# Optimization experiments

Hardware: AMD Instinct MI355X
Metric: run time of the kernel (lower is better)

Reference implementation:

```python
import math
import jax, jax.numpy as jnp
import numpy as np

B_SZ, N_TOK, D_INNER, S_STATE = 4, 1024, 384, 16
DT_MAX = 0.15


def setup_inputs() -> dict:
    key = jax.random.key(0)
    ks = jax.random.split(key, 10)
    dt_init = math.log(math.exp(0.1) - 1.0)  # softplus^-1(0.1)
    x = jax.random.normal(ks[0], (B_SZ, N_TOK, D_INNER), dtype=jnp.float32)
    dt_self_W = jax.random.uniform(ks[1], (D_INNER, D_INNER), minval=-1e-4, maxval=1e-4)
    dt_self_b = jnp.full((D_INNER,), dt_init, dtype=jnp.float32)
    dt_diff_W = jax.random.uniform(ks[2], (D_INNER, D_INNER), minval=-1e-4, maxval=1e-4)
    dt_diff_b = jnp.full((D_INNER,), dt_init, dtype=jnp.float32)
    B_W = jax.random.normal(ks[3], (D_INNER, S_STATE)) / math.sqrt(D_INNER)
    C_real_W = jax.random.normal(ks[4], (D_INNER, S_STATE)) / math.sqrt(D_INNER)
    C_imag_W = jax.random.normal(ks[5], (D_INNER, S_STATE)) / math.sqrt(D_INNER)
    D_param = jnp.ones((D_INNER,), dtype=jnp.float32)
    A_log = jnp.broadcast_to(jnp.log(jnp.arange(1, S_STATE + 1, dtype=jnp.float32))[None, :], (D_INNER, S_STATE))
    lap = jnp.array([[0.0, 1.0, 0.0], [1.0, -4.0, 1.0], [0.0, 1.0, 0.0]], dtype=jnp.float32) * 0.1
    conv_w = jnp.broadcast_to(lap[None, None], (D_INNER, 1, 3, 3)) + 0.01 * jax.random.normal(ks[6], (D_INNER, 1, 3, 3))
    reaction_alpha = 0.01 * jax.random.normal(ks[7], (1, 1, D_INNER, 1))
    reaction_beta = 0.01 * jax.random.normal(ks[8], (1, 1, D_INNER, 1))
    return {
        'x': x, 'dt_self_W': dt_self_W, 'dt_self_b': dt_self_b,
        'dt_diff_W': dt_diff_W, 'dt_diff_b': dt_diff_b,
        'B_W': B_W, 'C_real_W': C_real_W, 'C_imag_W': C_imag_W,
        'D_param': D_param, 'A_log': A_log, 'conv_w': conv_w,
        'reaction_alpha': reaction_alpha, 'reaction_beta': reaction_beta,
        'K_steps': 2,
    }


def _laplacian(h, conv_w, H, W):
    # h: (B, N, D, S) -> depthwise 3x3 conv with replicate pad over the HxW grid
    B, N, D, S = h.shape
    hs = h.transpose(0, 3, 2, 1).reshape(B * S, D, H, W)
    hp = jnp.pad(hs, ((0, 0), (0, 0), (1, 1), (1, 1)), mode='edge')
    lap = jax.lax.conv_general_dilated(
        hp, conv_w, window_strides=(1, 1), padding='VALID',
        feature_group_count=D, dimension_numbers=('NCHW', 'OIHW', 'NCHW'))
    return lap.reshape(B, S, D, N).transpose(0, 3, 2, 1)


def reference(x, dt_self_W, dt_self_b, dt_diff_W, dt_diff_b, B_W, C_real_W,
              C_imag_W, D_param, A_log, conv_w, reaction_alpha, reaction_beta,
              K_steps):
    B, N, D = x.shape
    H = Wg = int(math.sqrt(N))
    A = -jax.nn.softplus(A_log)  # (D, S)
    delta_s = jnp.minimum(jax.nn.softplus(x @ dt_self_W.T + dt_self_b), DT_MAX)[..., None]
    delta_d = jnp.minimum(jax.nn.softplus(x @ dt_diff_W.T + dt_diff_b), DT_MAX)[..., None]
    B_mat = x @ B_W          # (B, N, S)
    C_real = x @ C_real_W    # (B, N, S)
    C_imag = x @ C_imag_W    # (B, N, S)
    mamba_input = jnp.einsum('bnd,bns->bnds', x, B_mat)
    h_real = mamba_input
    h_imag = jnp.zeros_like(h_real)
    dt = 1.0 / K_steps
    A_exp = A[None, None]  # (1,1,D,S)
    for _ in range(K_steps):
        f1_real = delta_s * (A_exp * h_real + mamba_input)
        f1_imag = delta_s * (A_exp * h_imag)
        lap_real = _laplacian(h_real, conv_w, H, Wg)
        lap_imag = _laplacian(h_imag, conv_w, H, Wg)
        f2_real = delta_d * -lap_imag
        f2_imag = delta_d * lap_real
        reaction_scale = reaction_alpha - reaction_beta * (h_real ** 2 + h_imag ** 2)
        h_real = h_real + dt * (f1_real + f2_real + h_real * reaction_scale)
        h_imag = h_imag + dt * (f1_imag + f2_imag + h_imag * reaction_scale)
    y = (jnp.einsum('bnds,bns->bnd', h_real, C_real)
         + jnp.einsum('bnds,bns->bnd', h_imag, C_imag)
         + x * D_param)
    return y
```

## Files before the change

kernel.cpp:

```cpp
#include <hip/hip_runtime.h>
#include <hip/hip_fp16.h>
#include <math.h>

#define B_SZ    4
#define N_TOKC  1024
#define D_INNER 384
#define S_STATE 16
#define DT_MAX_V 0.15f
#define PLANE   (B_SZ * N_TOKC)
#define DN      ((size_t)B_SZ * D_INNER * N_TOKC)

typedef __attribute__((ext_vector_type(8))) short bf16x8;
typedef __attribute__((ext_vector_type(4))) float f32x4;

__device__ __forceinline__ float softplusf(float z) {
    return fmaxf(z, 0.f) + log1pf(expf(-fabsf(z)));
}

__device__ __forceinline__ unsigned short f2bf(float f) {
    unsigned u = __float_as_uint(f);
    unsigned r = (u + 0x7FFFu + ((u >> 16) & 1u)) >> 16;
    return (unsigned short)r;
}

__device__ __forceinline__ unsigned packh2(float a, float b) {
    __half2 h = __floats2half2_rn(a, b);
    union { __half2 h; unsigned u; } c; c.h = h; return c.u;
}
__device__ __forceinline__ __half2 uph2(unsigned u) {
    union { unsigned u; __half2 h; } c; c.u = u; return c.h;
}

__device__ __forceinline__ size_t frag_off(int T, int kb, int q, int l16) {
    return ((size_t)((T * 12 + kb) * 4 + q)) * 128 + l16 * 8;
}

__device__ __forceinline__ bf16x8 pack8(const float* v) {
    bf16x8 o;
#pragma unroll
    for (int e = 0; e < 8; e++) o[e] = (short)f2bf(v[e]);
    return o;
}

__global__ __launch_bounds__(256) void k_prep(
    const float* __restrict__ x, const float* __restrict__ Ws, const float* __restrict__ Wd,
    const float* __restrict__ BW, const float* __restrict__ CrW, const float* __restrict__ CiW,
    const float* __restrict__ A_log,
    float* __restrict__ x_t, unsigned short* __restrict__ xp,
    unsigned short* __restrict__ Wdtp, unsigned short* __restrict__ Wbcp,
    float* __restrict__ A_tab)
{
    const int t = threadIdx.x;
    const int bx = blockIdx.x;
    if (bx < 1536) {
        __shared__ __align__(16) float tile[32][36];
        const int tok0 = (bx & 127) * 32;
        const int d0   = (bx >> 7) * 32;
        const int b = tok0 >> 10, n0 = tok0 & 1023;
        {
            const int r = t >> 3, c4 = (t & 7) * 4;
            const float4 v = *(const float4*)(x + (size_t)(tok0 + r) * D_INNER + d0 + c4);
            tile[r][c4 + 0] = v.x; tile[r][c4 + 1] = v.y;
            tile[r][c4 + 2] = v.z; tile[r][c4 + 3] = v.w;
        }
        __syncthreads();
        {
            const int dr = t >> 3, n4 = (t & 7) * 4;
            float4 o;
            o.x = tile[n4 + 0][dr]; o.y = tile[n4 + 1][dr];
            o.z = tile[n4 + 2][dr]; o.w = tile[n4 + 3][dr];
            *(float4*)(x_t + ((size_t)(b * D_INNER + d0 + dr)) * N_TOKC + n0 + n4) = o;
        }
        if (t < 128) {
            const int tt = t >> 6, q = (t >> 4) & 3, l16 = t & 15;
            const int row = tt * 16 + l16;
            float v[8];
#pragma unroll
            for (int e = 0; e < 8; e++) v[e] = tile[row][q * 8 + e];
            *(bf16x8*)(xp + frag_off((tok0 >> 4) + tt, d0 >> 5, q, l16)) = pack8(v);
        }
    } else if (bx < 1584) {
        const int vv = bx - 1536;
        const int mat = vv >= 24;
        const int dt16 = mat ? vv - 24 : vv;
        const float* W = mat ? Wd : Ws;
        unsigned short* dst = Wdtp + (size_t)mat * 147456;
#pragma unroll
        for (int it = 0; it < 3; it++) {
            const int item = t + it * 256;
            const int l16 = item & 15, q = (item >> 4) & 3, kb = item >> 6;
            const float* src = W + (size_t)(dt16 * 16 + l16) * D_INNER + kb * 32 + q * 8;
            float v[8];
            const float4 v0 = *(const float4*)(src);
            const float4 v1 = *(const float4*)(src + 4);
            v[0] = v0.x; v[1] = v0.y; v[2] = v0.z; v[3] = v0.w;
            v[4] = v1.x; v[5] = v1.y; v[6] = v1.z; v[7] = v1.w;
            *(bf16x8*)(dst + frag_off(dt16, kb, q, l16)) = pack8(v);
        }
    } else if (bx < 1587) {
        const int m = bx - 1584;
        const float* W2 = (m == 0) ? BW : ((m == 1) ? CrW : CiW);
#pragma unroll
        for (int it = 0; it < 3; it++) {
            const int item = t + it * 256;
            const int l16 = item & 15, q = (item >> 4) & 3, kb = item >> 6;
            float v[8];
#pragma unroll
            for (int e = 0; e < 8; e++)
                v[e] = W2[(size_t)(kb * 32 + q * 8 + e) * S_STATE + l16];
            *(bf16x8*)(Wbcp + (size_t)m * 6144 + frag_off(0, kb, q, l16)) = pack8(v);
        }
    } else {
        for (int i = t; i < D_INNER * S_STATE; i += 256)
            A_tab[i] = -softplusf(A_log[i]);
    }
}

__global__ __launch_bounds__(256) void k_gemm(
    const unsigned short* __restrict__ xp, const unsigned short* __restrict__ Wdtp,
    const unsigned short* __restrict__ Wbcp,
    const float* __restrict__ bs, const float* __restrict__ bd,
    float* __restrict__ ds_t, float* __restrict__ dd_t,
    float* __restrict__ Bm_t, float* __restrict__ Cr_t, float* __restrict__ Ci_t)
{
    const int wave = threadIdx.x >> 6;
    const int lane = threadIdx.x & 63;
    const int quad = lane >> 4, l16 = lane & 15;

    if (blockIdx.x < 384) {
        const int dbase = (blockIdx.x >> 6) * 64;
        const int tbase = (blockIdx.x & 63) * 64;
        const int wd = (wave & 1) * 32;
        const int wt = (wave >> 1) * 32;
        const int dT0 = (dbase + wd) >> 4;
        const int tT0 = (tbase + wt) >> 4;

        f32x4 acc[2][2][2];
#pragma unroll
        for (int m = 0; m < 2; m++)
#pragma unroll
            for (int i = 0; i < 2; i++)
#pragma unroll
                for (int j = 0; j < 2; j++) acc[m][i][j] = (f32x4)0.f;

        bf16x8 a0[2][2], b0[2];
#pragma unroll
        for (int m = 0; m < 2; m++)
#pragma unroll
            for (int i = 0; i < 2; i++)
                a0[m][i] = *(const bf16x8*)(Wdtp + (size_t)m * 147456
                                            + frag_off(dT0 + i, 0, quad, l16));
#pragma unroll
        for (int j = 0; j < 2; j++)
            b0[j] = *(const bf16x8*)(xp + frag_off(tT0 + j, 0, quad, l16));

#pragma unroll 2
        for (int kb = 0; kb < 12; kb++) {
            bf16x8 a1[2][2], b1[2];
            const int kn = (kb < 11) ? kb + 1 : 11;
#pragma unroll
            for (int m = 0; m < 2; m++)
#pragma unroll
                for (int i = 0; i < 2; i++)
                    a1[m][i] = *(const bf16x8*)(Wdtp + (size_t)m * 147456
                                                + frag_off(dT0 + i, kn, quad, l16));
#pragma unroll
            for (int j = 0; j < 2; j++)
                b1[j] = *(const bf16x8*)(xp + frag_off(tT0 + j, kn, quad, l16));

#pragma unroll
            for (int m = 0; m < 2; m++)
#pragma unroll
                for (int i = 0; i < 2; i++)
#pragma unroll
                    for (int j = 0; j < 2; j++)
                        acc[m][i][j] = __builtin_amdgcn_mfma_f32_16x16x32_bf16(
                            a0[m][i], b0[j], acc[m][i][j], 0, 0, 0);

#pragma unroll
            for (int m = 0; m < 2; m++)
#pragma unroll
                for (int i = 0; i < 2; i++) a0[m][i] = a1[m][i];
#pragma unroll
            for (int j = 0; j < 2; j++) b0[j] = b1[j];
        }

#pragma unroll
        for (int m = 0; m < 2; m++) {
            const float* bias = (m == 0) ? bs : bd;
            float* out = (m == 0) ? ds_t : dd_t;
#pragma unroll
            for (int i = 0; i < 2; i++)
#pragma unroll
                for (int j = 0; j < 2; j++) {
                    const int tok = tbase + wt + j * 16 + l16;
                    const int bb = tok >> 10, n = tok & 1023;
#pragma unroll
                    for (int reg = 0; reg < 4; reg++) {
                        const int d = dbase + wd + i * 16 + quad * 4 + reg;
                        const float v = fminf(softplusf(acc[m][i][j][reg] + bias[d]), DT_MAX_V);
                        out[((size_t)(bb * D_INNER + d)) * N_TOKC + n] = v;
                    }
                }
        }
    } else {
        const int tT = (blockIdx.x - 384) * 4 + wave;
        f32x4 acc[3];
#pragma unroll
        for (int m = 0; m < 3; m++) acc[m] = (f32x4)0.f;

#pragma unroll 1
        for (int kb = 0; kb < 12; kb++) {
            const bf16x8 b = *(const bf16x8*)(xp + frag_off(tT, kb, quad, l16));
#pragma unroll
            for (int m = 0; m < 3; m++) {
                const bf16x8 a = *(const bf16x8*)(Wbcp + (size_t)m * 6144
                                                  + frag_off(0, kb, quad, l16));
                acc[m] = __builtin_amdgcn_mfma_f32_16x16x32_bf16(a, b, acc[m], 0, 0, 0);
            }
        }

        const int tok = tT * 16 + l16;
#pragma unroll
        for (int m = 0; m < 3; m++) {
            float* plane = (m == 0) ? Bm_t : ((m == 1) ? Cr_t : Ci_t);
#pragma unroll
            for (int reg = 0; reg < 4; reg++) {
                const int s = quad * 4 + reg;
                plane[(size_t)s * PLANE + tok] = acc[m][reg];
            }
        }
    }
}

#define PSTRIDE 33
#define PSIZE   (PSTRIDE * 32)

__global__ __launch_bounds__(256) void k_ssm(
    const float* __restrict__ x_t, const float* __restrict__ conv_w, const float* __restrict__ A_tab,
    const float* __restrict__ ralpha, const float* __restrict__ rbeta, const float* __restrict__ Dp,
    const float* __restrict__ ds_t, const float* __restrict__ dd_t,
    const float* __restrict__ Bm_t, const float* __restrict__ Cr_t, const float* __restrict__ Ci_t,
    float* __restrict__ y_part)
{
    const int sg = blockIdx.x;
    const int d  = blockIdx.y;
    const int b  = blockIdx.z;
    const int t  = threadIdx.x;
    const int c  = t & 31;
    const int g  = t >> 5;
    const int r0 = g * 4;

    __shared__ unsigned pl[4 * PSIZE];

    __half2 wh[9];
#pragma unroll
    for (int i = 0; i < 9; i++) wh[i] = __float2half2_rn(conv_w[d * 9 + i]);
    const float alpha = ralpha[d];
    const float beta  = rbeta[d];
    const float Dv    = Dp[d];
    float A[4];
#pragma unroll
    for (int s = 0; s < 4; s++) A[s] = A_tab[d * S_STATE + sg * 4 + s];

    const size_t base_dn = ((size_t)(b * D_INNER + d)) * N_TOKC;
    const size_t base_sn = (size_t)b * N_TOKC;

    float xv[4], dsv[4], ddv[4], u[4][4];
    float hr[4][4], hi[4][4];
#pragma unroll
    for (int k = 0; k < 4; k++) {
        const int n = (r0 + k) * 32 + c;
        xv[k]  = x_t [base_dn + n];
        dsv[k] = ds_t[base_dn + n];
        ddv[k] = dd_t[base_dn + n];
#pragma unroll
        for (int s = 0; s < 4; s++) {
            u[k][s]  = xv[k] * Bm_t[(size_t)(sg * 4 + s) * PLANE + base_sn + n];
            hr[k][s] = u[k][s];
        }
    }

    int tapw[6][3];
    {
        const int cm = (c > 0)  ? c - 1 : 0;
        const int cp = (c < 31) ? c + 1 : 31;
        const int rtop = (r0 > 0)  ? r0 - 1 : 0;
        const int rbot = (r0 < 28) ? r0 + 4 : 31;
        int rowb[6];
        rowb[0] = rtop * PSTRIDE;
#pragma unroll
        for (int k = 0; k < 4; k++) rowb[k + 1] = (r0 + k) * PSTRIDE;
        rowb[5] = rbot * PSTRIDE;
#pragma unroll
        for (int rr = 0; rr < 6; rr++) {
            tapw[rr][0] = rowb[rr] + cm;
            tapw[rr][1] = rowb[rr] + c;
            tapw[rr][2] = rowb[rr] + cp;
        }
    }
    const int ws0 = r0 * PSTRIDE + c;

#pragma unroll
    for (int p = 0; p < 2; p++)
#pragma unroll
        for (int k = 0; k < 4; k++)
            pl[p * PSIZE + ws0 + k * PSTRIDE] = packh2(hr[k][2 * p], hr[k][2 * p + 1]);
    __syncthreads();

#pragma unroll
    for (int p = 0; p < 2; p++) {
        __half2 tp[6][3];
#pragma unroll
        for (int rr = 0; rr < 6; rr++)
#pragma unroll
            for (int j = 0; j < 3; j++)
                tp[rr][j] = uph2(pl[p * PSIZE + tapw[rr][j]]);
#pragma unroll
        for (int k = 0; k < 4; k++) {
            __half2 ac = __float2half2_rn(0.f);
#pragma unroll
            for (int a = 0; a < 3; a++)
#pragma unroll
                for (int j = 0; j < 3; j++)
                    ac = __hfma2(wh[a * 3 + j], tp[k + a][j], ac);
            const float lap[2] = { __low2float(ac), __high2float(ac) };
#pragma unroll
            for (int e = 0; e < 2; e++) {
                const int s = 2 * p + e;
                const float hrv = hr[k][s];
                const float f1r = dsv[k] * fmaf(A[s], hrv, u[k][s]);
                const float rs  = fmaf(-beta, hrv * hrv, alpha);
                hr[k][s] = hrv + 0.5f * (f1r + hrv * rs);
                hi[k][s] = 0.5f * ddv[k] * lap[e];
            }
        }
    }
    __syncthreads();

#pragma unroll
    for (int s = 0; s < 4; s++)
#pragma unroll
        for (int k = 0; k < 4; k++)
            pl[s * PSIZE + ws0 + k * PSTRIDE] = packh2(hr[k][s], hi[k][s]);
    __syncthreads();

    float yp[4] = { 0.f, 0.f, 0.f, 0.f };
#pragma unroll
    for (int s = 0; s < 4; s++) {
        float crv[4], civ[4];
#pragma unroll
        for (int k = 0; k < 4; k++) {
            const size_t po = (size_t)(sg * 4 + s) * PLANE + base_sn + (r0 + k) * 32 + c;
            crv[k] = Cr_t[po];
            civ[k] = Ci_t[po];
        }
        __half2 tp[6][3];
#pragma unroll
        for (int rr = 0; rr < 6; rr++)
#pragma unroll
            for (int j = 0; j < 3; j++)
                tp[rr][j] = uph2(pl[s * PSIZE + tapw[rr][j]]);
#pragma unroll
        for (int k = 0; k < 4; k++) {
            __half2 ac = __float2half2_rn(0.f);
#pragma unroll
            for (int a = 0; a < 3; a++)
#pragma unroll
                for (int j = 0; j < 3; j++)
                    ac = __hfma2(wh[a * 3 + j], tp[k + a][j], ac);
            const float lapr = __low2float(ac);
            const float lapi = __high2float(ac);
            const float hrv = hr[k][s], hiv = hi[k][s];
            const float f1r = dsv[k] * fmaf(A[s], hrv, u[k][s]);
            const float f1i = dsv[k] * (A[s] * hiv);
            const float f2r = -ddv[k] * lapi;
            const float f2i =  ddv[k] * lapr;
            const float q   = fmaf(hrv, hrv, hiv * hiv);
            const float rs  = fmaf(-beta, q, alpha);
            const float nhr = hrv + 0.5f * (f1r + f2r + hrv * rs);
            const float nhi = hiv + 0.5f * (f1i + f2i + hiv * rs);
            yp[k] = fmaf(nhr, crv[k], yp[k]);
            yp[k] = fmaf(nhi, civ[k], yp[k]);
        }
    }

#pragma unroll
    for (int k = 0; k < 4; k++) {
        float v = yp[k];
        if (sg == 0) v = fmaf(xv[k], Dv, v);
        y_part[((size_t)((sg * B_SZ + b) * D_INNER + d)) * N_TOKC + (r0 + k) * 32 + c] = v;
    }
}

__global__ __launch_bounds__(256) void k_reduce(
    const float* __restrict__ y_part, float* __restrict__ y)
{
    const int d0 = blockIdx.x * 32;
    const int n0 = blockIdx.y * 32;
    const int b  = blockIdx.z;
    const int t  = threadIdx.x;
    __shared__ __align__(16) float tile[32][36];

    const int dr = t >> 3, nc4 = (t & 7) * 4;
    float4 acc = make_float4(0.f, 0.f, 0.f, 0.f);
#pragma unroll
    for (int sg = 0; sg < 4; sg++) {
        const float4 v = *(const float4*)(y_part
            + ((size_t)((sg * B_SZ + b) * D_INNER + d0 + dr)) * N_TOKC + n0 + nc4);
        acc.x += v.x; acc.y += v.y; acc.z += v.z; acc.w += v.w;
    }
    *(float4*)&tile[dr][nc4] = acc;
    __syncthreads();

    const int nr = t >> 3, dc4 = (t & 7) * 4;
    float4 o;
    o.x = tile[dc4 + 0][nr];
    o.y = tile[dc4 + 1][nr];
    o.z = tile[dc4 + 2][nr];
    o.w = tile[dc4 + 3][nr];
    *(float4*)(y + ((size_t)(b * N_TOKC + n0 + nr)) * D_INNER + d0 + dc4) = o;
}

extern "C" void kernel_launch(void* const* d_in, const int* in_sizes, int n_in,
                              void* d_out, int out_size, void* d_ws, size_t ws_size,
                              hipStream_t stream)
{
    const float* x    = (const float*)d_in[0];
    const float* Ws   = (const float*)d_in[1];
    const float* bsb  = (const float*)d_in[2];
    const float* Wd   = (const float*)d_in[3];
    const float* bdb  = (const float*)d_in[4];
    const float* BW   = (const float*)d_in[5];
    const float* CrW  = (const float*)d_in[6];
    const float* CiW  = (const float*)d_in[7];
    const float* Dp   = (const float*)d_in[8];
    const float* Alog = (const float*)d_in[9];
    const float* cw   = (const float*)d_in[10];
    const float* ra   = (const float*)d_in[11];
    const float* rb   = (const float*)d_in[12];
    float* y = (float*)d_out;

    float* ws     = (float*)d_ws;
    float* ds_t   = ws;
    float* dd_t   = ds_t + DN;
    float* x_t    = dd_t + DN;
    float* Bm_t   = x_t + DN;
    float* Cr_t   = Bm_t + (size_t)S_STATE * PLANE;
    float* Ci_t   = Cr_t + (size_t)S_STATE * PLANE;
    float* A_tab  = Ci_t + (size_t)S_STATE * PLANE;
    float* y_part = A_tab + (size_t)D_INNER * S_STATE;

    unsigned short* xp   = (unsigned short*)y_part;
    unsigned short* Wdtp = xp + (size_t)256 * 12 * 4 * 128;
    unsigned short* Wbcp = Wdtp + (size_t)2 * 147456;

    k_prep<<<dim3(1588), 256, 0, stream>>>(x, Ws, Wd, BW, CrW, CiW, Alog,
                                           x_t, xp, Wdtp, Wbcp, A_tab);
    k_gemm<<<dim3(448), 256, 0, stream>>>(xp, Wdtp, Wbcp, bsb, bdb,
                                          ds_t, dd_t, Bm_t, Cr_t, Ci_t);
    k_ssm<<<dim3(4, D_INNER, B_SZ), 256, 0, stream>>>(x_t, cw, A_tab, ra, rb, Dp,
                                                      ds_t, dd_t, Bm_t, Cr_t, Ci_t, y_part);
    k_reduce<<<dim3(12, 32, 4), 256, 0, stream>>>(y_part, y);
}
```

Baseline: 166.7 us.

## Pack dt and C projections to fp16 pairs and loop state groups inside SSM block

The GEMM epilogue now writes delta_s/delta_d and C_real/C_imag as packed half2 words instead of separate fp32 planes. This halves the intermediate traffic for those tensors. The SSM kernel now loops over the four state groups inside one block instead of launching one block per group. That removes the four-way partial y buffer, so the reduce kernel only transposes. The cost is fp16 precision on the dt and C values, and a grid four times smaller with a serial loop over groups per block.

```diff
diff --git a/kernel.cpp b/kernel.cpp
--- a/kernel.cpp
+++ b/kernel.cpp
@@ -120,8 +120,8 @@
     const unsigned short* __restrict__ xp, const unsigned short* __restrict__ Wdtp,
     const unsigned short* __restrict__ Wbcp,
     const float* __restrict__ bs, const float* __restrict__ bd,
-    float* __restrict__ ds_t, float* __restrict__ dd_t,
-    float* __restrict__ Bm_t, float* __restrict__ Cr_t, float* __restrict__ Ci_t)
+    unsigned* __restrict__ dsdd_t,
+    float* __restrict__ Bm_t, unsigned* __restrict__ cri_t)
 {
     const int wave = threadIdx.x >> 6;
     const int lane = threadIdx.x & 63;
@@ -186,23 +186,19 @@
         }
 
 #pragma unroll
-        for (int m = 0; m < 2; m++) {
-            const float* bias = (m == 0) ? bs : bd;
-            float* out = (m == 0) ? ds_t : dd_t;
-#pragma unroll
-            for (int i = 0; i < 2; i++)
-#pragma unroll
-                for (int j = 0; j < 2; j++) {
-                    const int tok = tbase + wt + j * 16 + l16;
-                    const int bb = tok >> 10, n = tok & 1023;
-#pragma unroll
-                    for (int reg = 0; reg < 4; reg++) {
-                        const int d = dbase + wd + i * 16 + quad * 4 + reg;
-                        const float v = fminf(softplusf(acc[m][i][j][reg] + bias[d]), DT_MAX_V);
-                        out[((size_t)(bb * D_INNER + d)) * N_TOKC + n] = v;
-                    }
+        for (int i = 0; i < 2; i++)
+#pragma unroll
+            for (int j = 0; j < 2; j++) {
+                const int tok = tbase + wt + j * 16 + l16;
+                const int bb = tok >> 10, n = tok & 1023;
+#pragma unroll
+                for (int reg = 0; reg < 4; reg++) {
+                    const int d = dbase + wd + i * 16 + quad * 4 + reg;
+                    const float vs = fminf(softplusf(acc[0][i][j][reg] + bs[d]), DT_MAX_V);
+                    const float vd = fminf(softplusf(acc[1][i][j][reg] + bd[d]), DT_MAX_V);
+                    dsdd_t[((size_t)(bb * D_INNER + d)) * N_TOKC + n] = packh2(vs, vd);
                 }
-        }
+            }
     } else {
         const int tT = (blockIdx.x - 384) * 4 + wave;
         f32x4 acc[3];
@@ -222,13 +218,10 @@
 
         const int tok = tT * 16 + l16;
 #pragma unroll
-        for (int m = 0; m < 3; m++) {
-            float* plane = (m == 0) ? Bm_t : ((m == 1) ? Cr_t : Ci_t);
-#pragma unroll
-            for (int reg = 0; reg < 4; reg++) {
-                const int s = quad * 4 + reg;
-                plane[(size_t)s * PLANE + tok] = acc[m][reg];
-            }
+        for (int reg = 0; reg < 4; reg++) {
+            const int s = quad * 4 + reg;
+            Bm_t [(size_t)s * PLANE + tok] = acc[0][reg];
+            cri_t[(size_t)s * PLANE + tok] = packh2(acc[1][reg], acc[2][reg]);
         }
     }
 }
@@ -239,13 +232,12 @@
 __global__ __launch_bounds__(256) void k_ssm(
     const float* __restrict__ x_t, const float* __restrict__ conv_w, const float* __restrict__ A_tab,
     const float* __restrict__ ralpha, const float* __restrict__ rbeta, const float* __restrict__ Dp,
-    const float* __restrict__ ds_t, const float* __restrict__ dd_t,
-    const float* __restrict__ Bm_t, const float* __restrict__ Cr_t, const float* __restrict__ Ci_t,
+    const unsigned* __restrict__ dsdd_t,
+    const float* __restrict__ Bm_t, const unsigned* __restrict__ cri_t,
     float* __restrict__ y_part)
 {
-    const int sg = blockIdx.x;
-    const int d  = blockIdx.y;
-    const int b  = blockIdx.z;
+    const int d  = blockIdx.x;
+    const int b  = blockIdx.y;
     const int t  = threadIdx.x;
     const int c  = t & 31;
     const int g  = t >> 5;
@@ -259,26 +251,18 @@
     const float alpha = ralpha[d];
     const float beta  = rbeta[d];
     const float Dv    = Dp[d];
-    float A[4];
-#pragma unroll
-    for (int s = 0; s < 4; s++) A[s] = A_tab[d * S_STATE + sg * 4 + s];
 
     const size_t base_dn = ((size_t)(b * D_INNER + d)) * N_TOKC;
     const size_t base_sn = (size_t)b * N_TOKC;
 
-    float xv[4], dsv[4], ddv[4], u[4][4];
-    float hr[4][4], hi[4][4];
+    float xv[4], dsv[4], ddv[4];
 #pragma unroll
     for (int k = 0; k < 4; k++) {
         const int n = (r0 + k) * 32 + c;
-        xv[k]  = x_t [base_dn + n];
-        dsv[k] = ds_t[base_dn + n];
-        ddv[k] = dd_t[base_dn + n];
-#pragma unroll
-        for (int s = 0; s < 4; s++) {
-            u[k][s]  = xv[k] * Bm_t[(size_t)(sg * 4 + s) * PLANE + base_sn + n];
-            hr[k][s] = u[k][s];
-        }
+        xv[k] = x_t[base_dn + n];
+        const __half2 dd = uph2(dsdd_t[base_dn + n]);
+        dsv[k] = __low2float(dd);
+        ddv[k] = __high2float(dd);
     }
 
     int tapw[6][3];
@@ -301,96 +285,109 @@
     }
     const int ws0 = r0 * PSTRIDE + c;
 
-#pragma unroll
-    for (int p = 0; p < 2; p++)
-#pragma unroll
-        for (int k = 0; k < 4; k++)
-            pl[p * PSIZE + ws0 + k * PSTRIDE] = packh2(hr[k][2 * p], hr[k][2 * p + 1]);
-    __syncthreads();
-
-#pragma unroll
-    for (int p = 0; p < 2; p++) {
-        __half2 tp[6][3];
-#pragma unroll
-        for (int rr = 0; rr < 6; rr++)
-#pragma unroll
-            for (int j = 0; j < 3; j++)
-                tp[rr][j] = uph2(pl[p * PSIZE + tapw[rr][j]]);
+    float yp[4] = { 0.f, 0.f, 0.f, 0.f };
+
+    for (int sg = 0; sg < 4; sg++) {
+        float A[4];
+#pragma unroll
+        for (int s = 0; s < 4; s++) A[s] = A_tab[d * S_STATE + sg * 4 + s];
+
+        float u[4][4], hr[4][4], hi[4][4];
 #pragma unroll
         for (int k = 0; k < 4; k++) {
-            __half2 ac = __float2half2_rn(0.f);
-#pragma unroll
-            for (int a = 0; a < 3; a++)
+            const int n = (r0 + k) * 32 + c;
+#pragma unroll
+            for (int s = 0; s < 4; s++) {
+                u[k][s]  = xv[k] * Bm_t[(size_t)(sg * 4 + s) * PLANE + base_sn + n];
+                hr[k][s] = u[k][s];
+            }
+        }
+
+#pragma unroll
+        for (int p = 0; p < 2; p++)
+#pragma unroll
+            for (int k = 0; k < 4; k++)
+                pl[p * PSIZE + ws0 + k * PSTRIDE] = packh2(hr[k][2 * p], hr[k][2 * p + 1]);
+        __syncthreads();
+
+#pragma unroll
+        for (int p = 0; p < 2; p++) {
+            __half2 tp[6][3];
+#pragma unroll
+            for (int rr = 0; rr < 6; rr++)
 #pragma unroll
                 for (int j = 0; j < 3; j++)
-                    ac = __hfma2(wh[a * 3 + j], tp[k + a][j], ac);
-            const float lap[2] = { __low2float(ac), __high2float(ac) };
-#pragma unroll
-            for (int e = 0; e < 2; e++) {
-                const int s = 2 * p + e;
-                const float hrv = hr[k][s];
+                    tp[rr][j] = uph2(pl[p * PSIZE + tapw[rr][j]]);
+#pragma unroll
+            for (int k = 0; k < 4; k++) {
+                __half2 ac = __float2half2_rn(0.f);
+#pragma unroll
+                for (int a = 0; a < 3; a++)
+#pragma unroll
+                    for (int j = 0; j < 3; j++)
+                        ac = __hfma2(wh[a * 3 + j], tp[k + a][j], ac);
+                const float lap[2] = { __low2float(ac), __high2float(ac) };
+#pragma unroll
+                for (int e = 0; e < 2; e++) {
+                    const int s = 2 * p + e;
+                    const float hrv = hr[k][s];
+                    const float f1r = dsv[k] * fmaf(A[s], hrv, u[k][s]);
+                    const float rs  = fmaf(-beta, hrv * hrv, alpha);
+                    hr[k][s] = hrv + 0.5f * (f1r + hrv * rs);
+                    hi[k][s] = 0.5f * ddv[k] * lap[e];
+                }
+            }
+        }
+        __syncthreads();
+
+#pragma unroll
+        for (int s = 0; s < 4; s++)
+#pragma unroll
+            for (int k = 0; k < 4; k++)
+                pl[s * PSIZE + ws0 + k * PSTRIDE] = packh2(hr[k][s], hi[k][s]);
+        __syncthreads();
+
+#pragma unroll
+        for (int s = 0; s < 4; s++) {
+            __half2 cri[4];
+#pragma unroll
+            for (int k = 0; k < 4; k++)
+                cri[k] = uph2(cri_t[(size_t)(sg * 4 + s) * PLANE + base_sn + (r0 + k) * 32 + c]);
+            __half2 tp[6][3];
+#pragma unroll
+            for (int rr = 0; rr < 6; rr++)
+#pragma unroll
+                for (int j = 0; j < 3; j++)
+                    tp[rr][j] = uph2(pl[s * PSIZE + tapw[rr][j]]);
+#pragma unroll
+            for (int k = 0; k < 4; k++) {
+                __half2 ac = __float2half2_rn(0.f);
+#pragma unroll
+                for (int a = 0; a < 3; a++)
+#pragma unroll
+                    for (int j = 0; j < 3; j++)
+                        ac = __hfma2(wh[a * 3 + j], tp[k + a][j], ac);
+                const float lapr = __low2float(ac);
+                const float lapi = __high2float(ac);
+                const float hrv = hr[k][s], hiv = hi[k][s];
                 const float f1r = dsv[k] * fmaf(A[s], hrv, u[k][s]);
-                const float rs  = fmaf(-beta, hrv * hrv, alpha);
-                hr[k][s] = hrv + 0.5f * (f1r + hrv * rs);
-                hi[k][s] = 0.5f * ddv[k] * lap[e];
+                const float f1i = dsv[k] * (A[s] * hiv);
+                const float f2r = -ddv[k] * lapi;
+                const float f2i =  ddv[k] * lapr;
+                const float q   = fmaf(hrv, hrv, hiv * hiv);
+                const float rs  = fmaf(-beta, q, alpha);
+                const float nhr = hrv + 0.5f * (f1r + f2r + hrv * rs);
+                const float nhi = hiv + 0.5f * (f1i + f2i + hiv * rs);
+                yp[k] = fmaf(nhr, __low2float(cri[k]), yp[k]);
+                yp[k] = fmaf(nhi, __high2float(cri[k]), yp[k]);
             }
         }
+        if (sg < 3) __syncthreads();
     }
-    __syncthreads();
-
-#pragma unroll
-    for (int s = 0; s < 4; s++)
-#pragma unroll
-        for (int k = 0; k < 4; k++)
-            pl[s * PSIZE + ws0 + k * PSTRIDE] = packh2(hr[k][s], hi[k][s]);
-    __syncthreads();
-
-    float yp[4] = { 0.f, 0.f, 0.f, 0.f };
-#pragma unroll
-    for (int s = 0; s < 4; s++) {
-        float crv[4], civ[4];
-#pragma unroll
-        for (int k = 0; k < 4; k++) {
-            const size_t po = (size_t)(sg * 4 + s) * PLANE + base_sn + (r0 + k) * 32 + c;
-            crv[k] = Cr_t[po];
-            civ[k] = Ci_t[po];
-        }
-        __half2 tp[6][3];
-#pragma unroll
-        for (int rr = 0; rr < 6; rr++)
-#pragma unroll
-            for (int j = 0; j < 3; j++)
-                tp[rr][j] = uph2(pl[s * PSIZE + tapw[rr][j]]);
-#pragma unroll
-        for (int k = 0; k < 4; k++) {
-            __half2 ac = __float2half2_rn(0.f);
-#pragma unroll
-            for (int a = 0; a < 3; a++)
-#pragma unroll
-                for (int j = 0; j < 3; j++)
-                    ac = __hfma2(wh[a * 3 + j], tp[k + a][j], ac);
-            const float lapr = __low2float(ac);
-            const float lapi = __high2float(ac);
-            const float hrv = hr[k][s], hiv = hi[k][s];
-            const float f1r = dsv[k] * fmaf(A[s], hrv, u[k][s]);
-            const float f1i = dsv[k] * (A[s] * hiv);
-            const float f2r = -ddv[k] * lapi;
-            const float f2i =  ddv[k] * lapr;
-            const float q   = fmaf(hrv, hrv, hiv * hiv);
-            const float rs  = fmaf(-beta, q, alpha);
-            const float nhr = hrv + 0.5f * (f1r + f2r + hrv * rs);
-            const float nhi = hiv + 0.5f * (f1i + f2i + hiv * rs);
-            yp[k] = fmaf(nhr, crv[k], yp[k]);
-            yp[k] = fmaf(nhi, civ[k], yp[k]);
-        }
-    }
-
-#pragma unroll
-    for (int k = 0; k < 4; k++) {
-        float v = yp[k];
-        if (sg == 0) v = fmaf(xv[k], Dv, v);
-        y_part[((size_t)((sg * B_SZ + b) * D_INNER + d)) * N_TOKC + (r0 + k) * 32 + c] = v;
-    }
+
+#pragma unroll
+    for (int k = 0; k < 4; k++)
+        y_part[base_dn + (r0 + k) * 32 + c] = fmaf(xv[k], Dv, yp[k]);
 }
 
 __global__ __launch_bounds__(256) void k_reduce(
@@ -403,14 +400,10 @@
     __shared__ __align__(16) float tile[32][36];
 
     const int dr = t >> 3, nc4 = (t & 7) * 4;
-    float4 acc = make_float4(0.f, 0.f, 0.f, 0.f);
-#pragma unroll
-    for (int sg = 0; sg < 4; sg++) {
-        const float4 v = *(const float4*)(y_part
-            + ((size_t)((sg * B_SZ + b) * D_INNER + d0 + dr)) * N_TOKC + n0 + nc4);
-        acc.x += v.x; acc.y += v.y; acc.z += v.z; acc.w += v.w;
-    }
-    *(float4*)&tile[dr][nc4] = acc;
+    const float4 v = *(const float4*)(y_part
+        + ((size_t)(b * D_INNER + d0 + dr)) * N_TOKC + n0 + nc4);
+    tile[dr][nc4 + 0] = v.x; tile[dr][nc4 + 1] = v.y;
+    tile[dr][nc4 + 2] = v.z; tile[dr][nc4 + 3] = v.w;
     __syncthreads();
 
     const int nr = t >> 3, dc4 = (t & 7) * 4;
@@ -441,25 +434,23 @@
     const float* rb   = (const float*)d_in[12];
     float* y = (float*)d_out;
 
-    float* ws     = (float*)d_ws;
-    float* ds_t   = ws;
-    float* dd_t   = ds_t + DN;
-    float* x_t    = dd_t + DN;
+    float* ws = (float*)d_ws;
+    unsigned* dsdd_t = (unsigned*)ws;
+    float* x_t    = ws + DN;
     float* Bm_t   = x_t + DN;
-    float* Cr_t   = Bm_t + (size_t)S_STATE * PLANE;
-    float* Ci_t   = Cr_t + (size_t)S_STATE * PLANE;
-    float* A_tab  = Ci_t + (size_t)S_STATE * PLANE;
+    unsigned* cri_t = (unsigned*)(Bm_t + (size_t)S_STATE * PLANE);
+    float* A_tab  = (float*)(cri_t + (size_t)S_STATE * PLANE);
     float* y_part = A_tab + (size_t)D_INNER * S_STATE;
 
-    unsigned short* xp   = (unsigned short*)y_part;
+    unsigned short* xp   = (unsigned short*)(y_part + DN);
     unsigned short* Wdtp = xp + (size_t)256 * 12 * 4 * 128;
     unsigned short* Wbcp = Wdtp + (size_t)2 * 147456;
 
     k_prep<<<dim3(1588), 256, 0, stream>>>(x, Ws, Wd, BW, CrW, CiW, Alog,
                                            x_t, xp, Wdtp, Wbcp, A_tab);
     k_gemm<<<dim3(448), 256, 0, stream>>>(xp, Wdtp, Wbcp, bsb, bdb,
-                                          ds_t, dd_t, Bm_t, Cr_t, Ci_t);
-    k_ssm<<<dim3(4, D_INNER, B_SZ), 256, 0, stream>>>(x_t, cw, A_tab, ra, rb, Dp,
-                                                      ds_t, dd_t, Bm_t, Cr_t, Ci_t, y_part);
+                                          dsdd_t, Bm_t, cri_t);
+    k_ssm<<<dim3(D_INNER, B_SZ), 256, 0, stream>>>(x_t, cw, A_tab, ra, rb, Dp,
+                                                   dsdd_t, Bm_t, cri_t, y_part);
     k_reduce<<<dim3(12, 32, 4), 256, 0, stream>>>(y_part, y);
 }
```

New measurement: 166.7 us. No clear change (+0.0%).
